# Kernel optimization log

Hardware: AMD Instinct MI355X
Metric: run time of the kernel (lower is better)

The kernel has to match this reference:

```python
import jax, jax.numpy as jnp
import numpy as np
from jax import lax

B, T, A, L, H, FD = 32, 64, 6, 32, 128, 256


def setup_inputs() -> dict:
    key = jax.random.key(0)
    ks = jax.random.split(key, 24)
    rn = lambda k, s, sc: jax.random.normal(k, s, jnp.float32) * sc
    return {
        "states": rn(ks[0], (B, T, 3, 64, 64), 1.0),
        "actions": rn(ks[1], (B, T, A), 1.0),
        # CNN encoder params (scale ~ 1/sqrt(fan_in))
        "c1_w": rn(ks[2], (32, 3, 4, 4), 0.14), "c1_b": rn(ks[3], (32,), 0.01),
        "c2_w": rn(ks[4], (64, 32, 4, 4), 0.044), "c2_b": rn(ks[5], (64,), 0.01),
        "c3_w": rn(ks[6], (128, 64, 4, 4), 0.031), "c3_b": rn(ks[7], (128,), 0.01),
        "c4_w": rn(ks[8], (256, 128, 4, 4), 0.022), "c4_b": rn(ks[9], (256,), 0.01),
        "fc_w": rn(ks[10], (FD, 256 * 4 * 4), 0.0156), "fc_b": rn(ks[11], (FD,), 0.01),
        # GRUCell params (torch layout: W_ih (3H, in), W_hh (3H, H))
        "gru_wih": rn(ks[12], (3 * H, L + A), 0.16), "gru_whh": rn(ks[13], (3 * H, H), 0.088),
        "gru_bih": rn(ks[14], (3 * H,), 0.01), "gru_bhh": rn(ks[15], (3 * H,), 0.01),
        "prior_w": rn(ks[16], (2 * L, H), 0.088), "prior_b": rn(ks[17], (2 * L,), 0.01),
        "post_w": rn(ks[18], (2 * L, H + FD), 0.05), "post_b": rn(ks[19], (2 * L,), 0.01),
        # reparameterization noise (randn_like in torch), one per (b, t)
        "eps": rn(ks[20], (B, T, L), 1.0),
    }


def _conv(x, w, b):
    # Conv2d(k=4, stride=2, pad=1), NCHW/OIHW
    y = lax.conv_general_dilated(x, w, window_strides=(2, 2),
                                 padding=[(1, 1), (1, 1)],
                                 dimension_numbers=("NCHW", "OIHW", "NCHW"))
    return jax.nn.relu(y + b[None, :, None, None])


def _encode(x, c1_w, c1_b, c2_w, c2_b, c3_w, c3_b, c4_w, c4_b, fc_w, fc_b):
    # x: (N, 3, 64, 64) -> (N, FD)
    x = _conv(x, c1_w, c1_b)
    x = _conv(x, c2_w, c2_b)
    x = _conv(x, c3_w, c3_b)
    x = _conv(x, c4_w, c4_b)  # (N, 256, 4, 4)
    x = x.reshape(x.shape[0], -1)
    return x @ fc_w.T + fc_b


def _gru_cell(x, h, wih, whh, bih, bhh):
    gi = x @ wih.T + bih
    gh = h @ whh.T + bhh
    i_r, i_z, i_n = jnp.split(gi, 3, axis=-1)
    h_r, h_z, h_n = jnp.split(gh, 3, axis=-1)
    r = jax.nn.sigmoid(i_r + h_r)
    z = jax.nn.sigmoid(i_z + h_z)
    n = jnp.tanh(i_n + r * h_n)
    return (1.0 - z) * n + z * h


def reference(states, actions, c1_w, c1_b, c2_w, c2_b, c3_w, c3_b, c4_w, c4_b,
              fc_w, fc_b, gru_wih, gru_whh, gru_bih, gru_bhh,
              prior_w, prior_b, post_w, post_b, eps):
    b, t = states.shape[0], states.shape[1]
    # encoder has no recurrent dependency: encode all frames at once
    feats = _encode(states.reshape(b * t, *states.shape[2:]),
                    c1_w, c1_b, c2_w, c2_b, c3_w, c3_b, c4_w, c4_b,
                    fc_w, fc_b).reshape(b, t, -1)  # (B, T, FD)

    def step(carry, inp):
        h, z = carry
        a_t, f_t, e_t = inp
        h = _gru_cell(jnp.concatenate([z, a_t], -1), h,
                      gru_wih, gru_whh, gru_bih, gru_bhh)
        mu_p, lv_p = jnp.split(h @ prior_w.T + prior_b, 2, axis=-1)
        mu_q, lv_q = jnp.split(jnp.concatenate([h, f_t], -1) @ post_w.T + post_b, 2, axis=-1)
        z = mu_q + jnp.exp(0.5 * lv_q) * e_t
        return (h, z), (mu_p, lv_p, mu_q, lv_q, h, z)

    h0 = jnp.zeros((b, gru_whh.shape[1]), states.dtype)
    z0 = jnp.zeros((b, prior_w.shape[0] // 2), states.dtype)
    xs = (jnp.swapaxes(actions, 0, 1), jnp.swapaxes(feats, 0, 1),
          jnp.swapaxes(eps, 0, 1))
    _, ys = lax.scan(step, (h0, z0), xs)
    # (T, B, d) -> (B, T, d)
    return tuple(jnp.swapaxes(y, 0, 1) for y in ys)
```

## Files before the change

kernel.cpp:

```cpp
#include <hip/hip_runtime.h>
#include <math.h>

#define Bn 32
#define Tn 64
#define An 6
#define Ln 32
#define Hn 128
#define FDn 256
#define Nimg (Bn*Tn)

typedef __attribute__((ext_vector_type(8))) short frag_ab;
typedef __attribute__((ext_vector_type(4))) float frag_cd;
typedef _Float16 h2_t __attribute__((ext_vector_type(2)));

__device__ __forceinline__ float sigmoid_fast(float x){
  return __builtin_amdgcn_rcpf(1.f + __expf(-x));
}
__device__ __forceinline__ float tanh_fast(float x){
  float x2 = fminf(fmaxf(2.f*x, -30.f), 30.f);
  float e = __expf(x2);
  return (e - 1.f) * __builtin_amdgcn_rcpf(e + 1.f);
}

__device__ __forceinline__ unsigned short f2bf(float f){
  unsigned int u = __float_as_uint(f);
  unsigned int r = (u + 0x7fffu + ((u >> 16) & 1u)) >> 16;
  return (unsigned short)r;
}
__device__ __forceinline__ unsigned packh(float a, float b){
  union { h2_t h; unsigned u; } x;
  x.h = (h2_t){(_Float16)a, (_Float16)b};
  return x.u;
}
__device__ __forceinline__ float fdot2u(unsigned a, unsigned b, float c){
  union { unsigned u; h2_t h; } ua, ub;
  ua.u = a; ub.u = b;
#if __has_builtin(__builtin_amdgcn_fdot2)
  return __builtin_amdgcn_fdot2(ua.h, ub.h, c, false);
#else
  return c + (float)ua.h.x*(float)ub.h.x + (float)ua.h.y*(float)ub.h.y;
#endif
}
#define BAR_LDS() asm volatile("s_waitcnt lgkmcnt(0)\n\ts_barrier" ::: "memory")

__global__ void __launch_bounds__(256)
states_nhwc_kernel(const float* __restrict__ src, unsigned short* __restrict__ dst)
{
  int idx = blockIdx.x*256 + threadIdx.x;
  int n = idx >> 12, pix = idx & 4095;
  const float* s = src + (size_t)n*3*4096 + pix;
  union { unsigned short e[4]; uint2 v; } u;
  u.e[0] = f2bf(s[0]); u.e[1] = f2bf(s[4096]); u.e[2] = f2bf(s[8192]); u.e[3] = 0;
  *(uint2*)(dst + (size_t)idx*4) = u.v;
}

#define WHH4_U 24576
#define PO4_U  (64*53*4)
#define SCAN_U (WHH4_U + PO4_U)

__global__ void __launch_bounds__(256)
prep2_kernel(const float* __restrict__ c1w, const float* __restrict__ c2w,
             const float* __restrict__ c3w, const float* __restrict__ c4w,
             const float* __restrict__ fcw,
             const float* __restrict__ gwhh, const float* __restrict__ gwih,
             const float* __restrict__ prw,  const float* __restrict__ pow_,
             unsigned short* __restrict__ w1p, unsigned short* __restrict__ w2p,
             unsigned short* __restrict__ w3p, unsigned short* __restrict__ w4p,
             unsigned short* __restrict__ wfcp,
             unsigned* __restrict__ g_scan, unsigned* __restrict__ g_wih2,
             unsigned* __restrict__ g_pr2)
{
  const int bid = blockIdx.x, tid = threadIdx.x;
  if (bid < 128){
    int idx = bid*256+tid;
    int k = idx >> 9, r = idx & 511, tap = r >> 5, c = r & 31;
    w2p[idx] = f2bf(c2w[k*512 + c*16 + tap]);
  } else if (bid < 640){
    int idx = (bid-128)*256+tid;
    int k = idx >> 10, r = idx & 1023, tap = r >> 6, c = r & 63;
    w3p[idx] = f2bf(c3w[k*1024 + c*16 + tap]);
  } else if (bid < 2688){
    int idx = (bid-640)*256+tid;
    int k = idx >> 11, r = idx & 2047, tap = r >> 7, c = r & 127;
    w4p[idx] = f2bf(c4w[k*2048 + c*16 + tap]);
  } else if (bid < 6784){
    int idx = (bid-2688)*256+tid;
    int o = idx >> 12, r = idx & 4095, sp = r >> 8, c = r & 255;
    wfcp[idx] = f2bf(fcw[o*4096 + c*16 + sp]);
  } else if (bid < 6792){
    int idx = (bid-6784)*256+tid;
    int k = idx >> 6, r = idx & 63, tap = r >> 2, c = r & 3;
    w1p[idx] = (c < 3) ? f2bf(c1w[k*48 + c*16 + tap]) : (unsigned short)0;
  } else if (bid < 6888){
    int idx = (bid-6792)*256+tid;
    int q = idx & 3, r2 = idx >> 2;
    int k8 = r2 / 384, i = r2 - k8*384;
    int k = 8*k8 + 2*q;
    g_scan[idx] = packh(gwhh[i*128 + k], gwhh[i*128 + k + 1]);
  } else if (bid < 6917){
    int idx = (bid-6888)*256+tid;
    if (idx < 19*384){
      int c = idx / 384, i = idx - c*384;
      g_wih2[idx] = packh(gwih[i*38 + 2*c], gwih[i*38 + 2*c + 1]);
    }
  } else if (bid < 6933){
    int idx = (bid-6917)*256+tid;
    int o = idx >> 6, c = idx & 63;
    g_pr2[idx] = packh(prw[o*128 + 2*c], prw[o*128 + 2*c + 1]);
  } else {
    int idx = (bid-6933)*256+tid;
    if (idx < 64*192){
      int o = idx / 192, r2 = idx - o*192;
      int u = r2 >> 2, q = r2 & 3;
      int j = u / 12, kk = u - j*12;
      int k = 96*j + 8*kk + 2*q;
      g_scan[WHH4_U + (o*53 + j*13 + kk)*4 + q] =
        packh(pow_[o*384 + k], pow_[o*384 + k + 1]);
    }
  }
}

template<int Cin, int IN, int Kout, int OUT, int BN, int LOG_SPB>
__global__ void __launch_bounds__(256)
convN_mfma(const unsigned short* __restrict__ in,
           const unsigned short* __restrict__ wB,
           const float* __restrict__ bias,
           unsigned short* __restrict__ out)
{
  constexpr int SPB = OUT*OUT;
  constexpr int KD  = 16*Cin;
  constexpr int NCH = KD/32;
  constexpr int NFN = BN/32;
  __shared__ __align__(16) unsigned short Alds[8*512];
  __shared__ __align__(16) unsigned short Blds[(BN/16)*512];

  const int tid = threadIdx.x;
  const int wave = tid >> 6, lane = tid & 63;
  const unsigned m0 = blockIdx.x * 128;
  const int n0 = blockIdx.y * BN;

  const int p = tid & 3;
  const unsigned short* baseA[2]; int oyA[2], oxA[2]; unsigned short* Adst[2];
#pragma unroll
  for (int h = 0; h < 2; h++){
    int r = (tid >> 2) + h*64;
    unsigned m = m0 + r;
    int nimg = m >> LOG_SPB;
    int sp = m & (SPB - 1);
    oyA[h] = sp / OUT; oxA[h] = sp & (OUT - 1);
    baseA[h] = in + (size_t)nimg * IN * IN * Cin;
    Adst[h] = &Alds[((r >> 4) << 9) + ((r & 15) << 3) + (p << 7)];
  }

  const int bn = tid >> 2, pb = tid & 3;
  const bool bAct = tid < BN*4;
  const unsigned short* Bsrc0 = wB + (size_t)(n0 + bn)*KD + pb*8;
  unsigned short* Bdst = &Blds[((bn >> 4) << 9) + ((bn & 15) << 3) + (pb << 7)];

  const int mhalf = wave >> 1, nhalf = wave & 1;
  frag_cd acc[4][NFN];
#pragma unroll
  for (int i = 0; i < 4; i++)
#pragma unroll
    for (int j = 0; j < NFN; j++) acc[i][j] = (frag_cd){0.f,0.f,0.f,0.f};

  auto loadA = [&](int kt, int h) -> uint4 {
    if constexpr (Cin >= 32){
      constexpr int CPT = Cin/32;
      int tap = kt / CPT;
      int c0 = (kt - tap*CPT)*32;
      int kh = tap >> 2, kw = tap & 3;
      int iy = 2*oyA[h] - 1 + kh;
      int ix = 2*oxA[h] - 1 + kw;
      uint4 v = {0u,0u,0u,0u};
      if ((unsigned)iy < (unsigned)IN && (unsigned)ix < (unsigned)IN)
        v = *(const uint4*)(baseA[h] + ((iy*IN + ix)*Cin + c0 + p*8));
      return v;
    } else {
      int kh = kt*2 + (p >> 1);
      int kw0 = (p & 1)*2;
      int iy = 2*oyA[h] - 1 + kh;
      int ix0 = 2*oxA[h] - 1 + kw0;
      union { uint2 u2[2]; uint4 u4; } v; v.u4 = (uint4){0u,0u,0u,0u};
      bool iyok = (unsigned)iy < (unsigned)IN;
      const unsigned short* rowp = baseA[h] + iy*IN*4;
#pragma unroll
      for (int d = 0; d < 2; d++){
        int ix = ix0 + d;
        if (iyok && (unsigned)ix < (unsigned)IN) v.u2[d] = *(const uint2*)(rowp + ix*4);
      }
      return v.u4;
    }
  };

  uint4 aPre0 = loadA(0,0), aPre1 = loadA(0,1);
  uint4 bPre = bAct ? *(const uint4*)Bsrc0 : (uint4){0u,0u,0u,0u};

#pragma unroll 1
  for (int kt = 0; kt < NCH; kt++){
    *(uint4*)Adst[0] = aPre0;
    *(uint4*)Adst[1] = aPre1;
    if (bAct) *(uint4*)Bdst = bPre;
    __syncthreads();
    if (kt + 1 < NCH){
      aPre0 = loadA(kt+1, 0);
      aPre1 = loadA(kt+1, 1);
      if (bAct) bPre = *(const uint4*)(Bsrc0 + (kt+1)*32);
    }
    frag_ab a[4], bf[NFN];
#pragma unroll
    for (int i = 0; i < 4; i++)
      a[i] = *(const frag_ab*)&Alds[(((mhalf<<2) + i) << 9) + lane*8];
#pragma unroll
    for (int j = 0; j < NFN; j++)
      bf[j] = *(const frag_ab*)&Blds[((nhalf*NFN + j) << 9) + lane*8];
#pragma unroll
    for (int i = 0; i < 4; i++)
#pragma unroll
      for (int j = 0; j < NFN; j++)
        acc[i][j] = __builtin_amdgcn_mfma_f32_16x16x32_bf16(a[i], bf[j], acc[i][j], 0, 0, 0);
    __syncthreads();
  }

  const unsigned mb = m0 + mhalf*64 + ((lane >> 4) << 2);
#pragma unroll
  for (int j = 0; j < NFN; j++){
    const int kg = n0 + nhalf*(NFN*16) + j*16 + (lane & 15);
    const float bv = bias[kg];
#pragma unroll
    for (int i = 0; i < 4; i++){
#pragma unroll
      for (int r = 0; r < 4; r++){
        unsigned mg = mb + i*16 + r;
        out[(size_t)mg*Kout + kg] = f2bf(fmaxf(acc[i][j][r] + bv, 0.f));
      }
    }
  }
}

__global__ void __launch_bounds__(256)
fc_mfma2(const unsigned short* __restrict__ A, const unsigned short* __restrict__ wB,
         const float* __restrict__ bias, float* __restrict__ outF)
{
  constexpr int KD = 4096, NCH = KD/32;
  __shared__ __align__(16) unsigned short Alds[4*512];
  __shared__ __align__(16) unsigned short Blds[4*512];

  const int tid = threadIdx.x, wave = tid >> 6, lane = tid & 63;
  const int m0 = blockIdx.x * 64, n0 = blockIdx.y * 64;
  const int r = tid >> 2, pc = tid & 3;
  const unsigned short* Asrc = A + (size_t)(m0 + r)*KD + pc*8;
  const unsigned short* Bsrc = wB + (size_t)(n0 + r)*KD + pc*8;
  unsigned short* Adst = &Alds[((r >> 4) << 9) + ((r & 15) << 3) + (pc << 7)];
  unsigned short* Bdst = &Blds[((r >> 4) << 9) + ((r & 15) << 3) + (pc << 7)];
  const int mh = wave >> 1, nh = wave & 1;

  frag_cd acc[2][2];
#pragma unroll
  for (int i = 0; i < 2; i++)
#pragma unroll
    for (int j = 0; j < 2; j++) acc[i][j] = (frag_cd){0.f,0.f,0.f,0.f};

  uint4 aP = *(const uint4*)Asrc, bP = *(const uint4*)Bsrc;
#pragma unroll 1
  for (int kt = 0; kt < NCH; kt++){
    *(uint4*)Adst = aP;
    *(uint4*)Bdst = bP;
    __syncthreads();
    if (kt + 1 < NCH){
      aP = *(const uint4*)(Asrc + (kt+1)*32);
      bP = *(const uint4*)(Bsrc + (kt+1)*32);
    }
    frag_ab a[2], b[2];
#pragma unroll
    for (int i = 0; i < 2; i++) a[i] = *(const frag_ab*)&Alds[(((mh<<1)+i) << 9) + lane*8];
#pragma unroll
    for (int j = 0; j < 2; j++) b[j] = *(const frag_ab*)&Blds[(((nh<<1)+j) << 9) + lane*8];
#pragma unroll
    for (int i = 0; i < 2; i++)
#pragma unroll
      for (int j = 0; j < 2; j++)
        acc[i][j] = __builtin_amdgcn_mfma_f32_16x16x32_bf16(a[i], b[j], acc[i][j], 0, 0, 0);
    __syncthreads();
  }

  const int mb = m0 + mh*32 + ((lane >> 4) << 2);
#pragma unroll
  for (int j = 0; j < 2; j++){
    const int kg = n0 + nh*32 + j*16 + (lane & 15);
    const float bv = bias[kg];
#pragma unroll
    for (int i = 0; i < 2; i++)
#pragma unroll
      for (int rr = 0; rr < 4; rr++)
        outF[(size_t)(mb + i*16 + rr)*256 + kg] = acc[i][j][rr] + bv;
  }
}

__global__ void __launch_bounds__(384)
rssm_scan4(const float* __restrict__ actions, const float* __restrict__ feats,
           const float* __restrict__ eps,
           const unsigned* __restrict__ g_scan,
           const unsigned* __restrict__ g_wih2,
           const unsigned* __restrict__ g_pr2,
           const float* __restrict__ bih,  const float* __restrict__ bhh,
           const float* __restrict__ prior_b, const float* __restrict__ post_b,
           float* __restrict__ out)
{
  __shared__ __align__(16) _Float16 sh_hfh[384];
  __shared__ __align__(16) _Float16 sh_xh[40];
  __shared__ __align__(16) float sh_gi[384];
  __shared__ __align__(16) float sh_gh[384];

  const int b = blockIdx.x, tid = threadIdx.x;

  uint4 whhr[16];
  {
    const uint4* src = (const uint4*)g_scan;
#pragma unroll
    for (int k8 = 0; k8 < 16; k8++) whhr[k8] = src[k8*384 + tid];
  }
  unsigned wih[19];
#pragma unroll
  for (int c = 0; c < 19; c++) wih[c] = g_wih2[c*384 + tid];

  unsigned prw[32];
  float prb = 0.f;
  if (tid < 128){
    const unsigned* src = g_pr2 + (tid >> 1)*64 + (tid & 1)*32;
#pragma unroll
    for (int c = 0; c < 32; c++) prw[c] = src[c];
    prb = prior_b[tid >> 1];
  }

  int om = 0, pj = 0, o_p = 0; bool is_mu = false; float pob = 0.f;
  uint4 pww[12];
  if (tid >= 128){
    const int tt = tid - 128;
    om = tt >> 2; pj = tt & 3;
    o_p = (om >> 1) + (om & 1)*32;
    is_mu = !(om & 1);
    pob = post_b[o_p];
    const uint4* src = (const uint4*)(g_scan + WHH4_U) + o_p*53 + pj*13;
#pragma unroll
    for (int kk = 0; kk < 12; kk++) pww[kk] = src[kk];
  }

  const float bih_i = bih[tid], bhh_i = bhh[tid];
  float hreg = 0.f;

  {
    const int bt0 = b*Tn;
    if (tid < Hn) sh_hfh[tid] = (_Float16)0.f;
    if (tid < Ln) sh_xh[tid] = (_Float16)0.f;
    if (tid >= 32 && tid < 38) sh_xh[tid] = (_Float16)actions[(size_t)bt0*An + (tid-32)];
    if (tid >= 64 && tid < 320) sh_hfh[128 + tid - 64] = (_Float16)feats[(size_t)bt0*FDn + (tid-64)];
  }
  __syncthreads();

  const uint4* H4   = (const uint4*)sh_hfh;
  const unsigned* X2 = (const unsigned*)sh_xh;

  const int OFF_MUP = 0;
  const int OFF_LVP = Bn*Tn*Ln;
  const int OFF_MUQ = 2*Bn*Tn*Ln;
  const int OFF_LVQ = 3*Bn*Tn*Ln;
  const int OFF_H   = 4*Bn*Tn*Ln;
  const int OFF_Z   = 4*Bn*Tn*Ln + Bn*Tn*Hn;

  float freg = 0.f, areg = 0.f, epsr = 0.f;

  for (int t = 0; t < Tn; t++){
    const int bt = b*Tn + t;

    if (t > 0 && tid >= 64 && tid < 320) sh_hfh[128 + tid - 64] = (_Float16)freg;
    if (t < Tn-1){
      if (tid >= 64 && tid < 320) freg = feats[(size_t)(bt+1)*FDn + (tid-64)];
      if (tid >= 320 && tid < 326) areg = actions[(size_t)(bt+1)*An + (tid-320)];
    }
    if (tid >= 128 && ((tid-128)&7) == 0) epsr = eps[(size_t)bt*Ln + ((tid-128)>>3)];

    {
      float a0 = bih_i, a1 = 0.f;
#pragma unroll
      for (int c = 0; c < 19; c += 2) a0 = fdot2u(wih[c], X2[c], a0);
#pragma unroll
      for (int c = 1; c < 19; c += 2) a1 = fdot2u(wih[c], X2[c], a1);
      sh_gi[tid] = a0 + a1;

      float g0 = bhh_i, g1 = 0.f, g2 = 0.f, g3 = 0.f;
#pragma unroll
      for (int k8 = 0; k8 < 16; k8++){
        uint4 w = whhr[k8];
        uint4 h = H4[k8];
        g0 = fdot2u(w.x, h.x, g0);
        g1 = fdot2u(w.y, h.y, g1);
        g2 = fdot2u(w.z, h.z, g2);
        g3 = fdot2u(w.w, h.w, g3);
      }
      sh_gh[tid] = (g0 + g1) + (g2 + g3);
    }
    BAR_LDS();

    if (tid < Hn){
      const float r  = sigmoid_fast(sh_gi[tid]       + sh_gh[tid]);
      const float zg = sigmoid_fast(sh_gi[Hn  + tid] + sh_gh[Hn  + tid]);
      const float nn = tanh_fast(fmaf(r, sh_gh[2*Hn + tid], sh_gi[2*Hn + tid]));
      hreg = (1.f - zg)*nn + zg*hreg;
      sh_hfh[tid] = (_Float16)hreg;
      out[OFF_H + (size_t)bt*Hn + tid] = hreg;
    }
    if (t < Tn-1 && tid >= 320 && tid < 326) sh_xh[32 + tid - 320] = (_Float16)areg;
    BAR_LDS();

    if (tid < 128){
      const int j = tid & 1;
      float a0 = 0.f, a1 = 0.f, a2 = 0.f, a3 = 0.f;
#pragma unroll
      for (int c4 = 0; c4 < 8; c4++){
        uint4 h = H4[8*j + c4];
        a0 = fdot2u(prw[4*c4+0], h.x, a0);
        a1 = fdot2u(prw[4*c4+1], h.y, a1);
        a2 = fdot2u(prw[4*c4+2], h.z, a2);
        a3 = fdot2u(prw[4*c4+3], h.w, a3);
      }
      float p = (a0 + a1) + (a2 + a3);
      p += __shfl_xor(p, 1);
      if (j == 0){
        const int o = tid >> 1;
        p += prb;
        if (o < Ln) out[OFF_MUP + (size_t)bt*Ln + o] = p;
        else        out[OFF_LVP + (size_t)bt*Ln + (o - Ln)] = p;
      }
    } else {
      float a0 = 0.f, a1 = 0.f, a2 = 0.f, a3 = 0.f;
#pragma unroll
      for (int kk = 0; kk < 12; kk++){
        uint4 w = pww[kk];
        uint4 h = H4[pj*12 + kk];
        a0 = fdot2u(w.x, h.x, a0);
        a1 = fdot2u(w.y, h.y, a1);
        a2 = fdot2u(w.z, h.z, a2);
        a3 = fdot2u(w.w, h.w, a3);
      }
      float p = (a0 + a1) + (a2 + a3);
      p += __shfl_xor(p, 1);
      p += __shfl_xor(p, 2);
      p += pob;
      const float q_part = __shfl_xor(p, 4);
      if (pj == 0){
        if (is_mu){
          const int o = om >> 1;
          out[OFF_MUQ + (size_t)bt*Ln + o] = p;
          const float zz = fmaf(__expf(0.5f*q_part), epsr, p);
          sh_xh[o] = (_Float16)zz;
          out[OFF_Z + (size_t)bt*Ln + o] = zz;
        } else {
          out[OFF_LVQ + (size_t)bt*Ln + (o_p - Ln)] = p;
        }
      }
    }
    BAR_LDS();
  }
}

extern "C" void kernel_launch(void* const* d_in, const int* in_sizes, int n_in,
                              void* d_out, int out_size, void* d_ws, size_t ws_size,
                              hipStream_t stream)
{
  const float* states = (const float*)d_in[0];
  const float* actions= (const float*)d_in[1];
  const float* c1_w = (const float*)d_in[2];  const float* c1_b = (const float*)d_in[3];
  const float* c2_w = (const float*)d_in[4];  const float* c2_b = (const float*)d_in[5];
  const float* c3_w = (const float*)d_in[6];  const float* c3_b = (const float*)d_in[7];
  const float* c4_w = (const float*)d_in[8];  const float* c4_b = (const float*)d_in[9];
  const float* fc_w = (const float*)d_in[10]; const float* fc_b = (const float*)d_in[11];
  const float* gwih = (const float*)d_in[12]; const float* gwhh = (const float*)d_in[13];
  const float* gbih = (const float*)d_in[14]; const float* gbhh = (const float*)d_in[15];
  const float* pr_w = (const float*)d_in[16]; const float* pr_b = (const float*)d_in[17];
  const float* po_w = (const float*)d_in[18]; const float* po_b = (const float*)d_in[19];
  const float* eps  = (const float*)d_in[20];

  char* p = (char*)d_ws;
  auto alloc = [&](size_t bytes){ char* r = p; p += (bytes + 255) & ~255ULL; return r; };

  unsigned short* statesB = (unsigned short*)alloc((size_t)Nimg*4096*4*2);
  unsigned short* act1    = (unsigned short*)alloc((size_t)Nimg*1024*32*2);
  unsigned short* act2    = (unsigned short*)alloc((size_t)Nimg*256*64*2);
  unsigned short* act3    = (unsigned short*)alloc((size_t)Nimg*64*128*2);
  unsigned short* act4    = (unsigned short*)alloc((size_t)Nimg*16*256*2);
  float*          feats   = (float*)alloc((size_t)Nimg*FDn*4);
  unsigned short* w1p     = (unsigned short*)alloc(32*64*2);
  unsigned short* w2p     = (unsigned short*)alloc((size_t)64*512*2);
  unsigned short* w3p     = (unsigned short*)alloc((size_t)128*1024*2);
  unsigned short* w4p     = (unsigned short*)alloc((size_t)256*2048*2);
  unsigned short* wfcp    = (unsigned short*)alloc((size_t)256*4096*2);
  unsigned* g_scan = (unsigned*)alloc((size_t)SCAN_U*4);
  unsigned* g_wih2 = (unsigned*)alloc((size_t)19*384*4);
  unsigned* g_pr2  = (unsigned*)alloc((size_t)64*64*4);

  states_nhwc_kernel<<<Nimg*4096/256, 256, 0, stream>>>(states, statesB);
  prep2_kernel<<<6981, 256, 0, stream>>>(c1_w, c2_w, c3_w, c4_w, fc_w,
                                         gwhh, gwih, pr_w, po_w,
                                         w1p, w2p, w3p, w4p, wfcp,
                                         g_scan, g_wih2, g_pr2);

  convN_mfma<4,64,32,32,32,10>  <<< dim3(Nimg*1024/128, 1), 256, 0, stream >>>(statesB, w1p, c1_b, act1);
  convN_mfma<32,32,64,16,64,8>  <<< dim3(Nimg*256/128, 1), 256, 0, stream >>>(act1, w2p, c2_b, act2);
  convN_mfma<64,16,128,8,64,6>  <<< dim3(Nimg*64/128, 2), 256, 0, stream >>>(act2, w3p, c3_b, act3);
  convN_mfma<128,8,256,4,64,4>  <<< dim3(Nimg*16/128, 4), 256, 0, stream >>>(act3, w4p, c4_b, act4);

  fc_mfma2<<< dim3(Nimg/64, 4), 256, 0, stream >>>(act4, wfcp, fc_b, feats);

  rssm_scan4<<< Bn, 384, 0, stream >>>(actions, feats, eps,
                                       g_scan, g_wih2, g_pr2,
                                       gbih, gbhh, pr_b, po_b, (float*)d_out);
}
```

Baseline: 664.2 us.

## Double-buffer LDS in conv and FC MFMA kernels with XOR-swizzled layout

Double-buffers the LDS A/B tiles in the conv and FC MFMA GEMMs, so writes for the next K-chunk overlap with MFMA on the current one and each iteration needs one barrier instead of two. It also adds an XOR swizzle to the LDS write and read offsets to cut bank conflicts. The plain __syncthreads is replaced with a lighter lgkmcnt wait plus barrier, and the loop is unrolled by two. The cost is twice the LDS per block, which may lower occupancy.

```diff
diff --git a/kernel.cpp b/kernel.cpp
--- a/kernel.cpp
+++ b/kernel.cpp
@@ -42,6 +42,13 @@
 #endif
 }
 #define BAR_LDS() asm volatile("s_waitcnt lgkmcnt(0)\n\ts_barrier" ::: "memory")
+
+__device__ __forceinline__ int swz_w(int r, int p){
+  return ((r >> 4) << 9) + (p << 7) + ((((r & 15) ^ (p << 2))) << 3);
+}
+__device__ __forceinline__ int swz_r(int f, int l){
+  return (f << 9) + ((l >> 4) << 7) + ((((l & 15) ^ ((l >> 4) << 2))) << 3);
+}
 
 __global__ void __launch_bounds__(256)
 states_nhwc_kernel(const float* __restrict__ src, unsigned short* __restrict__ dst)
@@ -131,8 +138,9 @@
   constexpr int KD  = 16*Cin;
   constexpr int NCH = KD/32;
   constexpr int NFN = BN/32;
-  __shared__ __align__(16) unsigned short Alds[8*512];
-  __shared__ __align__(16) unsigned short Blds[(BN/16)*512];
+  constexpr int BFR = BN/16;
+  __shared__ __align__(16) unsigned short Alds[2][8*512];
+  __shared__ __align__(16) unsigned short Blds[2][BFR*512];
 
   const int tid = threadIdx.x;
   const int wave = tid >> 6, lane = tid & 63;
@@ -140,7 +148,7 @@
   const int n0 = blockIdx.y * BN;
 
   const int p = tid & 3;
-  const unsigned short* baseA[2]; int oyA[2], oxA[2]; unsigned short* Adst[2];
+  const unsigned short* baseA[2]; int oyA[2], oxA[2]; int AdstI[2];
 #pragma unroll
   for (int h = 0; h < 2; h++){
     int r = (tid >> 2) + h*64;
@@ -149,13 +157,13 @@
     int sp = m & (SPB - 1);
     oyA[h] = sp / OUT; oxA[h] = sp & (OUT - 1);
     baseA[h] = in + (size_t)nimg * IN * IN * Cin;
-    Adst[h] = &Alds[((r >> 4) << 9) + ((r & 15) << 3) + (p << 7)];
+    AdstI[h] = swz_w(r, p);
   }
 
   const int bn = tid >> 2, pb = tid & 3;
   const bool bAct = tid < BN*4;
   const unsigned short* Bsrc0 = wB + (size_t)(n0 + bn)*KD + pb*8;
-  unsigned short* Bdst = &Blds[((bn >> 4) << 9) + ((bn & 15) << 3) + (pb << 7)];
+  const int BdstI = swz_w(bn, pb);
 
   const int mhalf = wave >> 1, nhalf = wave & 1;
   frag_cd acc[4][NFN];
@@ -193,33 +201,45 @@
     }
   };
 
-  uint4 aPre0 = loadA(0,0), aPre1 = loadA(0,1);
-  uint4 bPre = bAct ? *(const uint4*)Bsrc0 : (uint4){0u,0u,0u,0u};
-
-#pragma unroll 1
+  const int rdoff = swz_r(0, lane);
+
+  uint4 aR0 = loadA(0,0), aR1 = loadA(0,1);
+  uint4 bR = bAct ? *(const uint4*)Bsrc0 : (uint4){0u,0u,0u,0u};
+  *(uint4*)&Alds[0][AdstI[0]] = aR0;
+  *(uint4*)&Alds[0][AdstI[1]] = aR1;
+  if (bAct) *(uint4*)&Blds[0][BdstI] = bR;
+  if (NCH > 1){
+    aR0 = loadA(1,0); aR1 = loadA(1,1);
+    if (bAct) bR = *(const uint4*)(Bsrc0 + 32);
+  }
+  BAR_LDS();
+
+#pragma unroll 2
   for (int kt = 0; kt < NCH; kt++){
-    *(uint4*)Adst[0] = aPre0;
-    *(uint4*)Adst[1] = aPre1;
-    if (bAct) *(uint4*)Bdst = bPre;
-    __syncthreads();
+    const int cur = kt & 1, nxt = cur ^ 1;
     if (kt + 1 < NCH){
-      aPre0 = loadA(kt+1, 0);
-      aPre1 = loadA(kt+1, 1);
-      if (bAct) bPre = *(const uint4*)(Bsrc0 + (kt+1)*32);
+      *(uint4*)&Alds[nxt][AdstI[0]] = aR0;
+      *(uint4*)&Alds[nxt][AdstI[1]] = aR1;
+      if (bAct) *(uint4*)&Blds[nxt][BdstI] = bR;
+      if (kt + 2 < NCH){
+        aR0 = loadA(kt+2, 0);
+        aR1 = loadA(kt+2, 1);
+        if (bAct) bR = *(const uint4*)(Bsrc0 + (kt+2)*32);
+      }
     }
     frag_ab a[4], bf[NFN];
 #pragma unroll
     for (int i = 0; i < 4; i++)
-      a[i] = *(const frag_ab*)&Alds[(((mhalf<<2) + i) << 9) + lane*8];
+      a[i] = *(const frag_ab*)&Alds[cur][(((mhalf<<2) + i) << 9) + rdoff];
 #pragma unroll
     for (int j = 0; j < NFN; j++)
-      bf[j] = *(const frag_ab*)&Blds[((nhalf*NFN + j) << 9) + lane*8];
+      bf[j] = *(const frag_ab*)&Blds[cur][((nhalf*NFN + j) << 9) + rdoff];
 #pragma unroll
     for (int i = 0; i < 4; i++)
 #pragma unroll
       for (int j = 0; j < NFN; j++)
         acc[i][j] = __builtin_amdgcn_mfma_f32_16x16x32_bf16(a[i], bf[j], acc[i][j], 0, 0, 0);
-    __syncthreads();
+    BAR_LDS();
   }
 
   const unsigned mb = m0 + mhalf*64 + ((lane >> 4) << 2);
@@ -243,17 +263,17 @@
          const float* __restrict__ bias, float* __restrict__ outF)
 {
   constexpr int KD = 4096, NCH = KD/32;
-  __shared__ __align__(16) unsigned short Alds[4*512];
-  __shared__ __align__(16) unsigned short Blds[4*512];
+  __shared__ __align__(16) unsigned short Alds[2][4*512];
+  __shared__ __align__(16) unsigned short Blds[2][4*512];
 
   const int tid = threadIdx.x, wave = tid >> 6, lane = tid & 63;
   const int m0 = blockIdx.x * 64, n0 = blockIdx.y * 64;
   const int r = tid >> 2, pc = tid & 3;
   const unsigned short* Asrc = A + (size_t)(m0 + r)*KD + pc*8;
   const unsigned short* Bsrc = wB + (size_t)(n0 + r)*KD + pc*8;
-  unsigned short* Adst = &Alds[((r >> 4) << 9) + ((r & 15) << 3) + (pc << 7)];
-  unsigned short* Bdst = &Blds[((r >> 4) << 9) + ((r & 15) << 3) + (pc << 7)];
+  const int wI = swz_w(r, pc);
   const int mh = wave >> 1, nh = wave & 1;
+  const int rdoff = swz_r(0, lane);
 
   frag_cd acc[2][2];
 #pragma unroll
@@ -262,26 +282,34 @@
     for (int j = 0; j < 2; j++) acc[i][j] = (frag_cd){0.f,0.f,0.f,0.f};
 
   uint4 aP = *(const uint4*)Asrc, bP = *(const uint4*)Bsrc;
-#pragma unroll 1
+  *(uint4*)&Alds[0][wI] = aP;
+  *(uint4*)&Blds[0][wI] = bP;
+  aP = *(const uint4*)(Asrc + 32);
+  bP = *(const uint4*)(Bsrc + 32);
+  BAR_LDS();
+
+#pragma unroll 2
   for (int kt = 0; kt < NCH; kt++){
-    *(uint4*)Adst = aP;
-    *(uint4*)Bdst = bP;
-    __syncthreads();
+    const int cur = kt & 1, nxt = cur ^ 1;
     if (kt + 1 < NCH){
-      aP = *(const uint4*)(Asrc + (kt+1)*32);
-      bP = *(const uint4*)(Bsrc + (kt+1)*32);
+      *(uint4*)&Alds[nxt][wI] = aP;
+      *(uint4*)&Blds[nxt][wI] = bP;
+      if (kt + 2 < NCH){
+        aP = *(const uint4*)(Asrc + (kt+2)*32);
+        bP = *(const uint4*)(Bsrc + (kt+2)*32);
+      }
     }
     frag_ab a[2], b[2];
 #pragma unroll
-    for (int i = 0; i < 2; i++) a[i] = *(const frag_ab*)&Alds[(((mh<<1)+i) << 9) + lane*8];
-#pragma unroll
-    for (int j = 0; j < 2; j++) b[j] = *(const frag_ab*)&Blds[(((nh<<1)+j) << 9) + lane*8];
+    for (int i = 0; i < 2; i++) a[i] = *(const frag_ab*)&Alds[cur][(((mh<<1)+i) << 9) + rdoff];
+#pragma unroll
+    for (int j = 0; j < 2; j++) b[j] = *(const frag_ab*)&Blds[cur][(((nh<<1)+j) << 9) + rdoff];
 #pragma unroll
     for (int i = 0; i < 2; i++)
 #pragma unroll
       for (int j = 0; j < 2; j++)
         acc[i][j] = __builtin_amdgcn_mfma_f32_16x16x32_bf16(a[i], b[j], acc[i][j], 0, 0, 0);
-    __syncthreads();
+    BAR_LDS();
   }
 
   const int mb = m0 + mh*32 + ((lane >> 4) << 2);
```

New measurement: 621.4 us. -6.4%, faster.
